# Optimization experiments

Measured on AMD Instinct MI355X. Metric: run time of the kernel, lower is better.

The kernel has to match this reference:

```python
import jax, jax.numpy as jnp
import numpy as np

STRIDE, PAD, DIL = 1, 1, 1


def setup_inputs() -> dict:
    key = jax.random.key(0)
    ks = jax.random.split(key, 5)
    N, Cin, H, W = 8, 256, 56, 56
    Cout, kh, kw = 256, 3, 3
    x = jax.random.normal(ks[0], (N, Cin, H, W), jnp.float32)
    offset = jax.random.normal(ks[1], (N, 2 * kh * kw, H, W), jnp.float32)
    mask = jax.random.uniform(ks[2], (N, kh * kw, H, W), jnp.float32)
    fan_in = Cin * kh * kw
    bound = float(np.sqrt(6.0 / fan_in))  # kaiming_uniform, relu gain
    weight = jax.random.uniform(ks[3], (Cout, Cin, kh, kw), jnp.float32, -bound, bound)
    bias = jnp.zeros((Cout,), jnp.float32)
    return {"x": x, "offset": offset, "mask": mask, "weight": weight, "bias": bias}


def _mdcn(x, offset, mask, weight, bias):
    N, Cin, H, W = x.shape
    Cout, _, kh, kw = weight.shape
    K = kh * kw
    Hout = (H + 2 * PAD - (DIL * (kh - 1) + 1)) // STRIDE + 1
    Wout = (W + 2 * PAD - (DIL * (kw - 1) + 1)) // STRIDE + 1
    # offset channels: [K, 2(y,x)] interleaved -> [N,K,2,Hout,Wout]
    off = offset.reshape(N, K, 2, Hout, Wout)
    dy, dx = off[:, :, 0], off[:, :, 1]
    ky = (jnp.arange(K) // kw) * DIL
    kx = (jnp.arange(K) % kw) * DIL
    base_y = jnp.arange(Hout) * STRIDE - PAD
    base_x = jnp.arange(Wout) * STRIDE - PAD
    py = dy + ky[None, :, None, None] + base_y[None, None, :, None]  # [N,K,Ho,Wo]
    px = dx + kx[None, :, None, None] + base_x[None, None, None, :]
    y0 = jnp.floor(py)
    x0 = jnp.floor(px)
    wy1 = py - y0
    wx1 = px - x0
    wy0 = 1.0 - wy1
    wx0 = 1.0 - wx1
    y0i = y0.astype(jnp.int32)
    x0i = x0.astype(jnp.int32)
    x_nhwc = jnp.transpose(x, (0, 2, 3, 1))  # [N,H,W,Cin]
    nidx = jnp.arange(N)[:, None, None, None]

    def gather(yi, xi):
        valid = (yi >= 0) & (yi < H) & (xi >= 0) & (xi < W)
        yc = jnp.clip(yi, 0, H - 1)
        xc = jnp.clip(xi, 0, W - 1)
        v = x_nhwc[nidx, yc, xc]  # [N,K,Ho,Wo,Cin]
        return v * valid[..., None].astype(x.dtype)

    v = (gather(y0i, x0i) * (wy0 * wx0)[..., None]
         + gather(y0i, x0i + 1) * (wy0 * wx1)[..., None]
         + gather(y0i + 1, x0i) * (wy1 * wx0)[..., None]
         + gather(y0i + 1, x0i + 1) * (wy1 * wx1)[..., None])
    v = v * mask.reshape(N, K, Hout, Wout)[..., None]
    wr = weight.reshape(Cout, Cin, K)
    out = jnp.einsum('nkhwc,ock->nohw', v, wr)
    return out + bias[None, :, None, None]


def reference(x, offset, mask, weight, bias):
    return _mdcn(x, offset, mask, weight, bias)
```

## Files before the change

### kernel.cpp

```cpp
#include <hip/hip_runtime.h>
#include <math.h>

#define H_ 56
#define W_ 56
#define CIN 256
#define COUT 256
#define NB 8
#define SPIX 3136
#define KG 2304
#define MTOT 25088
#define MT 128
#define NBLK 196

typedef __bf16 v8bf __attribute__((ext_vector_type(8)));
typedef float  v4f  __attribute__((ext_vector_type(4)));

__device__ __forceinline__ void async_copy16(const void* g, void* l) {
    __builtin_amdgcn_global_load_lds(
        (const __attribute__((address_space(1))) void*)g,
        (__attribute__((address_space(3))) void*)l, 16, 0, 0);
}

__global__ __launch_bounds__(256) void prep_x(const float* __restrict__ x,
                                              __bf16* __restrict__ xb) {
    __shared__ float tile[64][65];
    const int n = blockIdx.z, c0 = blockIdx.y * 64, s0 = blockIdx.x * 64;
    const int tid = threadIdx.x;
    const float* xp = x + (size_t)n * CIN * SPIX;
    __bf16* xo = xb + (size_t)n * SPIX * CIN;
#pragma unroll
    for (int i = 0; i < 16; ++i) {
        int idx = tid + i * 256;
        int cr = idx >> 6, sc = idx & 63;
        tile[cr][sc] = xp[(c0 + cr) * SPIX + s0 + sc];
    }
    __syncthreads();
#pragma unroll
    for (int i = 0; i < 16; ++i) {
        int idx = tid + i * 256;
        int sr = idx >> 6, cc = idx & 63;
        xo[(s0 + sr) * CIN + c0 + cc] = (__bf16)tile[cc][sr];
    }
}

__global__ __launch_bounds__(256) void prep_w(const float* __restrict__ w,
                                              __bf16* __restrict__ bp) {
    const int i = blockIdx.x * 256 + threadIdx.x;
    if (i < COUT * KG) {
        const int o = i / KG;
        const int rem = i - o * KG;
        const int c = rem / 9;
        const int tap = rem - c * 9;
        bp[(size_t)o * KG + tap * 256 + c] = (__bf16)w[i];
    }
}

__device__ __forceinline__ void compute_params(
    const float* __restrict__ offs, const float* __restrict__ msk,
    int m0, int t0, int ntaps, int* sS, float4* sW, int tid)
{
    for (int idx = tid; idx < ntaps * MT; idx += 512) {
        const int tl = idx >> 7, pl = idx & 127;
        const int tap = t0 + tl;
        const int pg = m0 + pl;
        const int n  = pg / SPIX;
        const int s  = pg - n * SPIX;
        const int h  = s / W_, w = s - h * W_;
        const int kY = tap / 3, kX = tap - kY * 3;
        const float dy = offs[n * (18 * SPIX) + (2 * tap) * SPIX + s];
        const float dx = offs[n * (18 * SPIX) + (2 * tap + 1) * SPIX + s];
        const float mk = msk[n * (9 * SPIX) + tap * SPIX + s];
        const float py = dy + (float)(kY + h - 1);
        const float px = dx + (float)(kX + w - 1);
        const float fy0 = floorf(py), fx0 = floorf(px);
        const int y0 = (int)fy0, x0 = (int)fx0;
        const float wy1 = py - fy0, wx1 = px - fx0;
        const float wy0 = 1.f - wy1, wx0 = 1.f - wx1;
        const bool yv0 = (y0 >= 0) & (y0 < H_);
        const bool yv1 = (y0 + 1 >= 0) & (y0 + 1 < H_);
        const bool xv0 = (x0 >= 0) & (x0 < W_);
        const bool xv1 = (x0 + 1 >= 0) & (x0 + 1 < W_);
        float4 wt;
        wt.x = (yv0 & xv0) ? wy0 * wx0 * mk : 0.f;
        wt.y = (yv0 & xv1) ? wy0 * wx1 * mk : 0.f;
        wt.z = (yv1 & xv0) ? wy1 * wx0 * mk : 0.f;
        wt.w = (yv1 & xv1) ? wy1 * wx1 * mk : 0.f;
        sS[idx] = (n * SPIX + y0 * W_ + x0) * CIN;
        sW[idx] = wt;
    }
}

__global__ __launch_bounds__(512, 2) void mdcn_fused3(
    const __bf16* __restrict__ xb,
    const float*  __restrict__ offs,
    const float*  __restrict__ msk,
    const __bf16* __restrict__ bp,
    const float*  __restrict__ bias,
    float*        __restrict__ out)
{
    __shared__ __align__(16) char smem[61952];
    __bf16* As = (__bf16*)smem;
    __bf16* Bs = (__bf16*)(smem + 16384);
    int*    sS = (int*)(smem + 49152);
    float4* sW = (float4*)(smem + 51712);

    const int tid  = threadIdx.x;
    const int lane = tid & 63, wv = tid >> 6;
    const int wm = wv & 1, wn = wv >> 1;
    const int l15 = lane & 15, q = lane >> 4;

    const int xcd = blockIdx.x & 7, ib = blockIdx.x >> 3;
    const int wg  = (xcd < 4) ? xcd * 25 + ib : 100 + (xcd - 4) * 24 + ib;
    const int m0  = wg * MT;

    compute_params(offs, msk, m0, 0, 5, sS, sW, tid);

    v4f acc[4][4];
#pragma unroll
    for (int i = 0; i < 4; ++i)
#pragma unroll
        for (int j = 0; j < 4; ++j) acc[i][j] = (v4f)0.f;

    __syncthreads();

    const int pxl = tid >> 2, c2 = tid & 3;
    v8bf ga0, ga1, ga2, ga3, gb0, gb1, gb2, gb3;
    float4 cw;

#define GATHER(E, KQ)                                                   \
    { const int b_ = sS[E] + ((KQ) << 6) + c2 * 8;                      \
      cw  = sW[E];                                                      \
      ga0 = *(const v8bf*)(xb + b_);                                    \
      ga1 = *(const v8bf*)(xb + b_ + 256);                              \
      ga2 = *(const v8bf*)(xb + b_ + 14336);                            \
      ga3 = *(const v8bf*)(xb + b_ + 14592);                            \
      gb0 = *(const v8bf*)(xb + b_ + 32);                               \
      gb1 = *(const v8bf*)(xb + b_ + 288);                              \
      gb2 = *(const v8bf*)(xb + b_ + 14368);                            \
      gb3 = *(const v8bf*)(xb + b_ + 14624); }

    GATHER(pxl, 0)

#pragma unroll 1
    for (int ks = 0; ks < 36; ++ks) {
        v8bf r0, r1;
#pragma unroll
        for (int j = 0; j < 8; ++j) {
            r0[j] = (__bf16)(cw.x * (float)ga0[j] + cw.y * (float)ga1[j]
                           + cw.z * (float)ga2[j] + cw.w * (float)ga3[j]);
            r1[j] = (__bf16)(cw.x * (float)gb0[j] + cw.y * (float)gb1[j]
                           + cw.z * (float)gb2[j] + cw.w * (float)gb3[j]);
        }

        __syncthreads();

        *(v8bf*)(As + pxl * 64 + (((c2)     ^ (pxl & 7)) << 3)) = r0;
        *(v8bf*)(As + pxl * 64 + (((c2 + 4) ^ (pxl & 7)) << 3)) = r1;

        const int k0 = ks << 6;
#pragma unroll
        for (int t = 0; t < 4; ++t) {
            const int brow = t * 64 + (wv << 3) + (lane >> 3);
            const int blc  = (lane & 7) ^ (brow & 7);
            async_copy16(bp + (size_t)brow * KG + k0 + blc * 8,
                         smem + 16384 + ((t * 8 + wv) << 10));
        }

        if (ks == 19) {
            compute_params(offs, msk, m0, 5, 4, sS, sW, tid);
            __syncthreads();
        }

        if (ks < 35) {
            const int ks1 = ks + 1;
            const int tap = ks1 >> 2;
            const int e = (tap >= 5 ? tap - 5 : tap) * MT + pxl;
            GATHER(e, ks1 & 3)
        }

        __syncthreads();

#pragma unroll
        for (int kf = 0; kf < 2; ++kf) {
            v8bf afr[4], bfr[4];
#pragma unroll
            for (int mt = 0; mt < 4; ++mt) {
                const int row = wm * 64 + mt * 16 + l15;
                const int pch = (kf * 4 + q) ^ (row & 7);
                afr[mt] = *(const v8bf*)(As + row * 64 + pch * 8);
            }
#pragma unroll
            for (int nt = 0; nt < 4; ++nt) {
                const int row = wn * 64 + nt * 16 + l15;
                const int pch = (kf * 4 + q) ^ (row & 7);
                bfr[nt] = *(const v8bf*)(Bs + row * 64 + pch * 8);
            }
#pragma unroll
            for (int mt = 0; mt < 4; ++mt)
#pragma unroll
                for (int nt = 0; nt < 4; ++nt)
                    acc[mt][nt] = __builtin_amdgcn_mfma_f32_16x16x32_bf16(
                        afr[mt], bfr[nt], acc[mt][nt], 0, 0, 0);
        }
    }
#undef GATHER

    __syncthreads();
    float* epi = (float*)smem + wv * 1104;
    const int pg_l = m0 + wm * 64 + lane;
    const int n_l  = pg_l / SPIX;
    float* outp = out + (size_t)n_l * (COUT * SPIX) + (pg_l - n_l * SPIX);

#pragma unroll
    for (int nt = 0; nt < 4; ++nt) {
        const float bv = bias[wn * 64 + nt * 16 + l15];
#pragma unroll
        for (int mt = 0; mt < 4; ++mt)
#pragma unroll
            for (int r = 0; r < 4; ++r)
                epi[(mt * 16 + q * 4 + r) * 17 + l15] = acc[mt][nt][r] + bv;
#pragma unroll
        for (int oc = 0; oc < 16; ++oc)
            outp[(size_t)(wn * 64 + nt * 16 + oc) * SPIX] = epi[lane * 17 + oc];
    }
}

#define BM 64
#define BN 64
#define BKF 32
#define AST 68
#define BST 68
#define CST 65
__global__ __launch_bounds__(256) void mdcn_fallback(
    const float* __restrict__ xs, const float* __restrict__ offs,
    const float* __restrict__ msk, const float* __restrict__ wraw,
    const float* __restrict__ bias, float* __restrict__ out)
{
    __shared__ float smem[BKF * AST + BKF * BST];
    __shared__ int   sBase[4][BM];
    __shared__ float sWgt[4][BM];
    float (*At)[AST] = (float (*)[AST])smem;
    float (*Bt)[BST] = (float (*)[BST])(smem + BKF * AST);
    float (*Cs)[CST] = (float (*)[CST])smem;
    const int tid = threadIdx.x;
    const int m0 = blockIdx.x * BM;
    const int o0 = blockIdx.y * BN;
    const int n  = m0 / SPIX;
    const int s0 = m0 - n * SPIX;
    const int tx = tid & 15, ty = tid >> 4;
    float acc[4][4] = {};
    for (int k = 0; k < 9; ++k) {
        if (tid < BM) {
            const int s = s0 + tid;
            const int h = s / W_;
            const int w = s - h * W_;
            const int kY = k / 3, kX = k - kY * 3;
            const float dy = offs[(size_t)n * (18 * SPIX) + (size_t)(2 * k) * SPIX + s];
            const float dx = offs[(size_t)n * (18 * SPIX) + (size_t)(2 * k + 1) * SPIX + s];
            const float mk = msk[(size_t)n * (9 * SPIX) + (size_t)k * SPIX + s];
            const float py = dy + (float)(kY + h - 1);
            const float px = dx + (float)(kX + w - 1);
            const float fy0 = floorf(py), fx0 = floorf(px);
            const int y0 = (int)fy0, x0 = (int)fx0;
            const float wy1 = py - fy0, wx1 = px - fx0;
            const float wy0 = 1.0f - wy1, wx0 = 1.0f - wx1;
#pragma unroll
            for (int t = 0; t < 4; ++t) {
                const int yi = y0 + (t >> 1), xi = x0 + (t & 1);
                const bool valid = (yi >= 0) & (yi < H_) & (xi >= 0) & (xi < W_);
                const int yc = min(max(yi, 0), H_ - 1);
                const int xc = min(max(xi, 0), W_ - 1);
                float wt = ((t >> 1) ? wy1 : wy0) * ((t & 1) ? wx1 : wx0) * mk;
                sBase[t][tid] = n * (CIN * SPIX) + yc * W_ + xc;
                sWgt[t][tid] = valid ? wt : 0.0f;
            }
        }
        __syncthreads();
        for (int c0 = 0; c0 < CIN; c0 += BKF) {
#pragma unroll
            for (int i = 0; i < 8; ++i) {
                int idx = tid + i * 256;
                int row = idx >> 5, cc = idx & 31;
                int ce = (c0 + cc) * SPIX;
                At[cc][row] = sWgt[0][row] * xs[sBase[0][row] + ce]
                            + sWgt[1][row] * xs[sBase[1][row] + ce]
                            + sWgt[2][row] * xs[sBase[2][row] + ce]
                            + sWgt[3][row] * xs[sBase[3][row] + ce];
            }
#pragma unroll
            for (int i = 0; i < 8; ++i) {
                int idx = tid + i * 256;
                int kf = idx >> 6, o = idx & 63;
                Bt[kf][o] = wraw[(size_t)(o0 + o) * KG + (c0 + kf) * 9 + k];
            }
            __syncthreads();
#pragma unroll
            for (int kf = 0; kf < BKF; ++kf) {
                const float4 a = *(const float4*)&At[kf][ty * 4];
                const float4 b = *(const float4*)&Bt[kf][tx * 4];
                acc[0][0] = fmaf(a.x, b.x, acc[0][0]); acc[0][1] = fmaf(a.x, b.y, acc[0][1]);
                acc[0][2] = fmaf(a.x, b.z, acc[0][2]); acc[0][3] = fmaf(a.x, b.w, acc[0][3]);
                acc[1][0] = fmaf(a.y, b.x, acc[1][0]); acc[1][1] = fmaf(a.y, b.y, acc[1][1]);
                acc[1][2] = fmaf(a.y, b.z, acc[1][2]); acc[1][3] = fmaf(a.y, b.w, acc[1][3]);
                acc[2][0] = fmaf(a.z, b.x, acc[2][0]); acc[2][1] = fmaf(a.z, b.y, acc[2][1]);
                acc[2][2] = fmaf(a.z, b.z, acc[2][2]); acc[2][3] = fmaf(a.z, b.w, acc[2][3]);
                acc[3][0] = fmaf(a.w, b.x, acc[3][0]); acc[3][1] = fmaf(a.w, b.y, acc[3][1]);
                acc[3][2] = fmaf(a.w, b.z, acc[3][2]); acc[3][3] = fmaf(a.w, b.w, acc[3][3]);
            }
            __syncthreads();
        }
    }
#pragma unroll
    for (int i = 0; i < 4; ++i)
#pragma unroll
        for (int j = 0; j < 4; ++j)
            Cs[ty * 4 + i][tx * 4 + j] = acc[i][j] + bias[o0 + tx * 4 + j];
    __syncthreads();
    const int pix = tid & 63, ob = tid >> 6;
    float* outp = out + (size_t)n * COUT * SPIX + s0 + pix;
#pragma unroll
    for (int r = 0; r < 16; ++r) {
        int o = r * 4 + ob;
        outp[(size_t)(o0 + o) * SPIX] = Cs[pix][o];
    }
}

extern "C" void kernel_launch(void* const* d_in, const int* in_sizes, int n_in,
                              void* d_out, int out_size, void* d_ws, size_t ws_size,
                              hipStream_t stream) {
    const float* x    = (const float*)d_in[0];
    const float* offs = (const float*)d_in[1];
    const float* msk  = (const float*)d_in[2];
    const float* w    = (const float*)d_in[3];
    const float* bias = (const float*)d_in[4];
    float* out = (float*)d_out;

    const size_t GUARD    = (size_t)4 << 20;
    const size_t xb_bytes = (size_t)NB * SPIX * CIN * sizeof(__bf16);
    const size_t bp_bytes = (size_t)KG * COUT * sizeof(__bf16);
    const size_t need     = GUARD + xb_bytes + GUARD + bp_bytes;

    if (ws_size >= need) {
        __bf16* xb = (__bf16*)((char*)d_ws + GUARD);
        __bf16* bp = (__bf16*)((char*)d_ws + GUARD + xb_bytes + GUARD);
        prep_x<<<dim3(49, 4, 8), 256, 0, stream>>>(x, xb);
        prep_w<<<dim3((COUT * KG + 255) / 256), 256, 0, stream>>>(w, bp);
        mdcn_fused3<<<dim3(NBLK), 512, 0, stream>>>(xb, offs, msk, bp, bias, out);
    } else {
        mdcn_fallback<<<dim3(MTOT / BM, COUT / BN), 256, 0, stream>>>(
            x, offs, msk, w, bias, out);
    }
}
```

Baseline: 162.8 us.

## Double-buffer A/B tiles with gather two steps ahead and merge prep kernels

```diff
diff --git a/kernel.cpp b/kernel.cpp
--- a/kernel.cpp
+++ b/kernel.cpp
@@ -11,9 +11,16 @@
 #define MTOT 25088
 #define MT 128
 #define NBLK 196
+#define GUARD_PX 2048
 
 typedef __bf16 v8bf __attribute__((ext_vector_type(8)));
 typedef float  v4f  __attribute__((ext_vector_type(4)));
+
+#define WAIT_VM(N)  do { asm volatile("s_waitcnt vmcnt(" #N ")" ::: "memory"); \
+                         __builtin_amdgcn_sched_barrier(0); } while (0)
+#define WAIT_LGKM0  do { asm volatile("s_waitcnt lgkmcnt(0)" ::: "memory"); \
+                         __builtin_amdgcn_sched_barrier(0); } while (0)
+#define BARR        do { asm volatile("s_barrier" ::: "memory"); } while (0)
 
 __device__ __forceinline__ void async_copy16(const void* g, void* l) {
     __builtin_amdgcn_global_load_lds(
@@ -21,55 +28,55 @@
         (__attribute__((address_space(3))) void*)l, 16, 0, 0);
 }
 
-__global__ __launch_bounds__(256) void prep_x(const float* __restrict__ x,
-                                              __bf16* __restrict__ xb) {
+__global__ __launch_bounds__(256) void prep_xw(const float* __restrict__ x,
+                                               const float* __restrict__ w,
+                                               __bf16* __restrict__ xb,
+                                               __bf16* __restrict__ bp) {
     __shared__ float tile[64][65];
-    const int n = blockIdx.z, c0 = blockIdx.y * 64, s0 = blockIdx.x * 64;
     const int tid = threadIdx.x;
-    const float* xp = x + (size_t)n * CIN * SPIX;
-    __bf16* xo = xb + (size_t)n * SPIX * CIN;
-#pragma unroll
-    for (int i = 0; i < 16; ++i) {
-        int idx = tid + i * 256;
-        int cr = idx >> 6, sc = idx & 63;
-        tile[cr][sc] = xp[(c0 + cr) * SPIX + s0 + sc];
-    }
-    __syncthreads();
-#pragma unroll
-    for (int i = 0; i < 16; ++i) {
-        int idx = tid + i * 256;
-        int sr = idx >> 6, cc = idx & 63;
-        xo[(s0 + sr) * CIN + c0 + cc] = (__bf16)tile[cc][sr];
-    }
-}
-
-__global__ __launch_bounds__(256) void prep_w(const float* __restrict__ w,
-                                              __bf16* __restrict__ bp) {
-    const int i = blockIdx.x * 256 + threadIdx.x;
-    if (i < COUT * KG) {
-        const int o = i / KG;
-        const int rem = i - o * KG;
-        const int c = rem / 9;
-        const int tap = rem - c * 9;
-        bp[(size_t)o * KG + tap * 256 + c] = (__bf16)w[i];
+    if (blockIdx.z < 8) {
+        const int n = blockIdx.z, c0 = blockIdx.y * 64, s0 = blockIdx.x * 64;
+        const float* xp = x + (size_t)n * CIN * SPIX;
+        __bf16* xo = xb + (size_t)n * SPIX * CIN;
+#pragma unroll
+        for (int i = 0; i < 16; ++i) {
+            int idx = tid + i * 256;
+            int cr = idx >> 6, sc = idx & 63;
+            tile[cr][sc] = xp[(c0 + cr) * SPIX + s0 + sc];
+        }
+        __syncthreads();
+#pragma unroll
+        for (int i = 0; i < 16; ++i) {
+            int idx = tid + i * 256;
+            int sr = idx >> 6, cc = idx & 63;
+            xo[(s0 + sr) * CIN + c0 + cc] = (__bf16)tile[cc][sr];
+        }
+    } else {
+        const int base = (blockIdx.y * 49 + blockIdx.x) * 256 + tid;
+        for (int i = base; i < COUT * KG; i += 196 * 256) {
+            const int o = i / KG;
+            const int rem = i - o * KG;
+            const int c = rem / 9;
+            const int tap = rem - c * 9;
+            bp[(size_t)o * KG + tap * 256 + c] = (__bf16)w[i];
+        }
     }
 }
 
 __device__ __forceinline__ void compute_params(
     const float* __restrict__ offs, const float* __restrict__ msk,
-    int m0, int t0, int ntaps, int* sS, float4* sW, int tid)
+    int m0, int* sS, float4* sW, int tid)
 {
-    for (int idx = tid; idx < ntaps * MT; idx += 512) {
+    for (int idx = tid; idx < 9 * MT; idx += 512) {
         const int tl = idx >> 7, pl = idx & 127;
-        const int tap = t0 + tl;
         const int pg = m0 + pl;
         const int n  = pg / SPIX;
         const int s  = pg - n * SPIX;
         const int h  = s / W_, w = s - h * W_;
-        const int kY = tap / 3, kX = tap - kY * 3;
-        const float dy = offs[n * (18 * SPIX) + (2 * tap) * SPIX + s];
-        const float dx = offs[n * (18 * SPIX) + (2 * tap + 1) * SPIX + s];
-        const float mk = msk[n * (9 * SPIX) + tap * SPIX + s];
+        const int kY = tl / 3, kX = tl - kY * 3;
+        const float dy = offs[n * (18 * SPIX) + (2 * tl) * SPIX + s];
+        const float dx = offs[n * (18 * SPIX) + (2 * tl + 1) * SPIX + s];
+        const float mk = msk[n * (9 * SPIX) + tl * SPIX + s];
         const float py = dy + (float)(kY + h - 1);
         const float px = dx + (float)(kX + w - 1);
         const float fy0 = floorf(py), fx0 = floorf(px);
@@ -85,12 +92,14 @@
         wt.y = (yv0 & xv1) ? wy0 * wx1 * mk : 0.f;
         wt.z = (yv1 & xv0) ? wy1 * wx0 * mk : 0.f;
         wt.w = (yv1 & xv1) ? wy1 * wx1 * mk : 0.f;
-        sS[idx] = (n * SPIX + y0 * W_ + x0) * CIN;
+        int base = n * SPIX + y0 * W_ + x0;
+        base = min(max(base, -GUARD_PX), NB * SPIX - 58 + GUARD_PX);
+        sS[idx] = base * CIN;
         sW[idx] = wt;
     }
 }
 
-__global__ __launch_bounds__(512, 2) void mdcn_fused3(
+__global__ __launch_bounds__(512, 2) void mdcn_fused4(
     const __bf16* __restrict__ xb,
     const float*  __restrict__ offs,
     const float*  __restrict__ msk,
@@ -98,11 +107,9 @@
     const float*  __restrict__ bias,
     float*        __restrict__ out)
 {
-    __shared__ __align__(16) char smem[61952];
-    __bf16* As = (__bf16*)smem;
-    __bf16* Bs = (__bf16*)(smem + 16384);
-    int*    sS = (int*)(smem + 49152);
-    float4* sW = (float4*)(smem + 51712);
+    __shared__ __align__(16) char smem[121344];
+    int*    sS = (int*)(smem + 98304);
+    float4* sW = (float4*)(smem + 102912);
 
     const int tid  = threadIdx.x;
     const int lane = tid & 63, wv = tid >> 6;
@@ -113,7 +120,7 @@
     const int wg  = (xcd < 4) ? xcd * 25 + ib : 100 + (xcd - 4) * 24 + ib;
     const int m0  = wg * MT;
 
-    compute_params(offs, msk, m0, 0, 5, sS, sW, tid);
+    compute_params(offs, msk, m0, sS, sW, tid);
 
     v4f acc[4][4];
 #pragma unroll
@@ -139,47 +146,50 @@
       gb2 = *(const v8bf*)(xb + b_ + 14368);                            \
       gb3 = *(const v8bf*)(xb + b_ + 14624); }
 
+#define COMBINE_STORE(AP)                                               \
+    { v8bf r0, r1;                                                      \
+      _Pragma("unroll")                                                 \
+      for (int j = 0; j < 8; ++j) {                                     \
+        r0[j] = (__bf16)(cw.x * (float)ga0[j] + cw.y * (float)ga1[j]    \
+                       + cw.z * (float)ga2[j] + cw.w * (float)ga3[j]);  \
+        r1[j] = (__bf16)(cw.x * (float)gb0[j] + cw.y * (float)gb1[j]    \
+                       + cw.z * (float)gb2[j] + cw.w * (float)gb3[j]);  \
+      }                                                                 \
+      *(v8bf*)((AP) + pxl * 64 + (((c2)     ^ (pxl & 7)) << 3)) = r0;   \
+      *(v8bf*)((AP) + pxl * 64 + (((c2 + 4) ^ (pxl & 7)) << 3)) = r1; }
+
+#define STAGE_B(K0, LB)                                                 \
+    { _Pragma("unroll")                                                 \
+      for (int t = 0; t < 4; ++t) {                                     \
+        const int brow = t * 64 + (wv << 3) + (lane >> 3);              \
+        const int blc  = (lane & 7) ^ (brow & 7);                       \
+        async_copy16(bp + (size_t)brow * KG + (K0) + blc * 8,           \
+                     (LB) + ((t * 8 + wv) << 10)); }
+
     GATHER(pxl, 0)
+    COMBINE_STORE((__bf16*)smem)
+    STAGE_B(0, smem + 32768) }
+    GATHER(pxl, 1)
+    WAIT_LGKM0;
+    WAIT_VM(8);
+    BARR;
+
+    char* ac = smem;          char* an = smem + 16384;
+    char* bc = smem + 32768;  char* bn = smem + 65536;
 
 #pragma unroll 1
     for (int ks = 0; ks < 36; ++ks) {
-        v8bf r0, r1;
-#pragma unroll
-        for (int j = 0; j < 8; ++j) {
-            r0[j] = (__bf16)(cw.x * (float)ga0[j] + cw.y * (float)ga1[j]
-                           + cw.z * (float)ga2[j] + cw.w * (float)ga3[j]);
-            r1[j] = (__bf16)(cw.x * (float)gb0[j] + cw.y * (float)gb1[j]
-                           + cw.z * (float)gb2[j] + cw.w * (float)gb3[j]);
-        }
-
-        __syncthreads();
-
-        *(v8bf*)(As + pxl * 64 + (((c2)     ^ (pxl & 7)) << 3)) = r0;
-        *(v8bf*)(As + pxl * 64 + (((c2 + 4) ^ (pxl & 7)) << 3)) = r1;
-
-        const int k0 = ks << 6;
-#pragma unroll
-        for (int t = 0; t < 4; ++t) {
-            const int brow = t * 64 + (wv << 3) + (lane >> 3);
-            const int blc  = (lane & 7) ^ (brow & 7);
-            async_copy16(bp + (size_t)brow * KG + k0 + blc * 8,
-                         smem + 16384 + ((t * 8 + wv) << 10));
-        }
-
-        if (ks == 19) {
-            compute_params(offs, msk, m0, 5, 4, sS, sW, tid);
-            __syncthreads();
-        }
-
         if (ks < 35) {
-            const int ks1 = ks + 1;
-            const int tap = ks1 >> 2;
-            const int e = (tap >= 5 ? tap - 5 : tap) * MT + pxl;
-            GATHER(e, ks1 & 3)
-        }
-
-        __syncthreads();
-
+            STAGE_B((ks + 1) << 6, bn) }
+            WAIT_VM(4);
+            COMBINE_STORE((__bf16*)an)
+            if (ks < 34) {
+                const int st = ks + 2;
+                GATHER((st >> 2) * MT + pxl, st & 3)
+            }
+        }
+
+        __builtin_amdgcn_s_setprio(1);
 #pragma unroll
         for (int kf = 0; kf < 2; ++kf) {
             v8bf afr[4], bfr[4];
@@ -187,13 +197,13 @@
             for (int mt = 0; mt < 4; ++mt) {
                 const int row = wm * 64 + mt * 16 + l15;
                 const int pch = (kf * 4 + q) ^ (row & 7);
-                afr[mt] = *(const v8bf*)(As + row * 64 + pch * 8);
+                afr[mt] = *(const v8bf*)((__bf16*)ac + row * 64 + pch * 8);
             }
 #pragma unroll
             for (int nt = 0; nt < 4; ++nt) {
                 const int row = wn * 64 + nt * 16 + l15;
                 const int pch = (kf * 4 + q) ^ (row & 7);
-                bfr[nt] = *(const v8bf*)(Bs + row * 64 + pch * 8);
+                bfr[nt] = *(const v8bf*)((__bf16*)bc + row * 64 + pch * 8);
             }
 #pragma unroll
             for (int mt = 0; mt < 4; ++mt)
@@ -202,10 +212,27 @@
                     acc[mt][nt] = __builtin_amdgcn_mfma_f32_16x16x32_bf16(
                         afr[mt], bfr[nt], acc[mt][nt], 0, 0, 0);
         }
+        __builtin_amdgcn_s_setprio(0);
+
+        if (ks < 34) {
+            WAIT_LGKM0;
+            WAIT_VM(8);
+            BARR;
+        } else if (ks == 34) {
+            WAIT_LGKM0;
+            WAIT_VM(0);
+            BARR;
+        }
+        char* t;
+        t = ac; ac = an; an = t;
+        t = bc; bc = bn; bn = t;
     }
 #undef GATHER
-
-    __syncthreads();
+#undef COMBINE_STORE
+#undef STAGE_B
+
+    WAIT_LGKM0;
+    BARR;
     float* epi = (float*)smem + wv * 1104;
     const int pg_l = m0 + wm * 64 + lane;
     const int n_l  = pg_l / SPIX;
@@ -335,17 +362,18 @@
     const float* bias = (const float*)d_in[4];
     float* out = (float*)d_out;
 
-    const size_t GUARD    = (size_t)4 << 20;
+    const size_t GUARD_B  = (size_t)GUARD_PX * CIN * sizeof(__bf16);
     const size_t xb_bytes = (size_t)NB * SPIX * CIN * sizeof(__bf16);
     const size_t bp_bytes = (size_t)KG * COUT * sizeof(__bf16);
-    const size_t need     = GUARD + xb_bytes + GUARD + bp_bytes;
+    const size_t need     = GUARD_B + xb_bytes + GUARD_B + bp_bytes;
 
     if (ws_size >= need) {
-        __bf16* xb = (__bf16*)((char*)d_ws + GUARD);
-        __bf16* bp = (__bf16*)((char*)d_ws + GUARD + xb_bytes + GUARD);
-        prep_x<<<dim3(49, 4, 8), 256, 0, stream>>>(x, xb);
-        prep_w<<<dim3((COUT * KG + 255) / 256), 256, 0, stream>>>(w, bp);
-        mdcn_fused3<<<dim3(NBLK), 512, 0, stream>>>(xb, offs, msk, bp, bias, out);
+        __bf16* xb = (__bf16*)((char*)d_ws + GUARD_B);
+        __bf16* bp = (__bf16*)((char*)d_ws + GUARD_B + xb_bytes + GUARD_B);
+        hipMemsetAsync(d_ws, 0, GUARD_B, stream);
+        hipMemsetAsync((char*)d_ws + GUARD_B + xb_bytes, 0, GUARD_B, stream);
+        prep_xw<<<dim3(49, 4, 9), 256, 0, stream>>>(x, w, xb, bp);
+        mdcn_fused4<<<dim3(NBLK), 512, 0, stream>>>(xb, offs, msk, bp, bias, out);
     } else {
         mdcn_fallback<<<dim3(MTOT / BM, COUT / BN), 256, 0, stream>>>(
             x, offs, msk, w, bias, out);
```

Result: faster. 156.0 us (-4.2%).
